# Kernel tuning notes

Hardware: AMD Instinct MI355X
Metric: run time of the kernel (lower is better)

## Reference

```python
import jax, jax.numpy as jnp
import numpy as np


def setup_inputs() -> dict:
    key = jax.random.key(0)
    k1, k2 = jax.random.split(key)
    B, C, N = 32, 512, 4096
    x = jax.random.normal(k1, (B, C, N), dtype=jnp.float32)
    gamma = jax.random.normal(k2, (1,), dtype=jnp.float32)
    return {"x": x, "gamma": gamma}


def reference(x, gamma):
    # x: [B, C, N]. Channel attention: energy = x @ x^T -> [B, C, C]
    energy = jnp.einsum('bcn,bdn->bcd', x, x)
    # inverted score: rowmax - energy, then softmax over last dim
    energy_new = jnp.max(energy, axis=-1, keepdims=True) - energy
    attention = jax.nn.softmax(energy_new, axis=-1)  # [B, C, C]
    out = jnp.einsum('bcd,bdn->bcn', attention, x)
    return gamma * out + x
```

## Files before the change

### kernel.cpp

```cpp
#include <hip/hip_runtime.h>
#include <stdint.h>
#include <stddef.h>

#define NB 32
#define NC 512
#define NN 4096
#define NSPLIT 4
#define KCH (NN / NSPLIT)

typedef _Float16 h4_t __attribute__((ext_vector_type(4)));
typedef _Float16 h8_t __attribute__((ext_vector_type(8)));
typedef float    f4_t __attribute__((ext_vector_type(4)));

__device__ __forceinline__ void gload16(const _Float16* g, _Float16* l) {
    __builtin_amdgcn_global_load_lds(
        (const __attribute__((address_space(1))) void*)g,
        (__attribute__((address_space(3))) void*)l, 16, 0, 0);
}

__global__ __launch_bounds__(256) void cast_hl(
    const float* __restrict__ x, _Float16* __restrict__ Xh,
    _Float16* __restrict__ Xl)
{
    const size_t total = (size_t)NB * NC * NN / 4;
    for (size_t i = (size_t)blockIdx.x * 256 + threadIdx.x; i < total;
         i += (size_t)gridDim.x * 256) {
        const float4 v = ((const float4*)x)[i];
        const _Float16 h0 = (_Float16)v.x, h1 = (_Float16)v.y;
        const _Float16 h2 = (_Float16)v.z, h3 = (_Float16)v.w;
        h4_t hv = {h0, h1, h2, h3};
        h4_t lv = {(_Float16)(v.x - (float)h0), (_Float16)(v.y - (float)h1),
                   (_Float16)(v.z - (float)h2), (_Float16)(v.w - (float)h3)};
        ((h4_t*)Xh)[i] = hv;
        ((h4_t*)Xl)[i] = lv;
    }
}

__global__ __launch_bounds__(256, 4) void gemm1_energy(
    const _Float16* __restrict__ Xh, const _Float16* __restrict__ Xl,
    float* __restrict__ part)
{
    __shared__ __attribute__((aligned(16))) _Float16 sAh[128 * 32];
    __shared__ __attribute__((aligned(16))) _Float16 sBh[128 * 32];
    __shared__ __attribute__((aligned(16))) _Float16 sAl[128 * 32];
    __shared__ __attribute__((aligned(16))) _Float16 sBl[128 * 32];

    const int flat = blockIdx.x;
    const int xcd  = flat & 7;
    const int slot = flat >> 3;
    const int grp  = xcd + 8 * (slot / 10);
    const int mem  = slot % 10;
    const int b    = grp >> 2;
    const int s    = grp & (NSPLIT - 1);

    const int ti = (int)((sqrtf(8.0f * (float)mem + 1.0f) - 1.0f) * 0.5f);
    const int tj = mem - ((ti * (ti + 1)) >> 1);

    const int t = threadIdx.x;
    const int wave = t >> 6, lane = t & 63;
    const int srow = t >> 2, scol = (t & 3) * 8;

    const size_t xb = (size_t)b * NC * NN + (size_t)s * KCH;
    const _Float16* gAh = Xh + xb + (size_t)(ti * 128 + srow) * NN + scol;
    const _Float16* gBh = Xh + xb + (size_t)(tj * 128 + srow) * NN + scol;
    const _Float16* gAl = Xl + xb + (size_t)(ti * 128 + srow) * NN + scol;
    const _Float16* gBl = Xl + xb + (size_t)(tj * 128 + srow) * NN + scol;

    const int wr = wave >> 1, wc = wave & 1;
    const int fr = lane & 15, fko = (lane >> 4) * 8;

    f4_t acc[4][4];
#pragma unroll
    for (int m = 0; m < 4; ++m)
#pragma unroll
        for (int n = 0; n < 4; ++n) acc[m][n] = (f4_t){0.f, 0.f, 0.f, 0.f};

    for (int k0 = 0; k0 < KCH; k0 += 32) {
        gload16(gAh + k0,                   sAh + wave * 512);
        gload16(gAh + k0 + 64 * (size_t)NN, sAh + 2048 + wave * 512);
        gload16(gBh + k0,                   sBh + wave * 512);
        gload16(gBh + k0 + 64 * (size_t)NN, sBh + 2048 + wave * 512);
        gload16(gAl + k0,                   sAl + wave * 512);
        gload16(gAl + k0 + 64 * (size_t)NN, sAl + 2048 + wave * 512);
        gload16(gBl + k0,                   sBl + wave * 512);
        gload16(gBl + k0 + 64 * (size_t)NN, sBl + 2048 + wave * 512);
        __syncthreads();

        h8_t ah[4], bh[4], al[4], bl[4];
#pragma unroll
        for (int m = 0; m < 4; ++m) {
            ah[m] = *(const h8_t*)(sAh + (wr * 64 + m * 16 + fr) * 32 + fko);
            bh[m] = *(const h8_t*)(sBh + (wc * 64 + m * 16 + fr) * 32 + fko);
            al[m] = *(const h8_t*)(sAl + (wr * 64 + m * 16 + fr) * 32 + fko);
            bl[m] = *(const h8_t*)(sBl + (wc * 64 + m * 16 + fr) * 32 + fko);
        }
#pragma unroll
        for (int m = 0; m < 4; ++m)
#pragma unroll
            for (int n = 0; n < 4; ++n) {
                acc[m][n] = __builtin_amdgcn_mfma_f32_16x16x32_f16(ah[m], bh[n], acc[m][n], 0, 0, 0);
                acc[m][n] = __builtin_amdgcn_mfma_f32_16x16x32_f16(ah[m], bl[n], acc[m][n], 0, 0, 0);
                acc[m][n] = __builtin_amdgcn_mfma_f32_16x16x32_f16(al[m], bh[n], acc[m][n], 0, 0, 0);
            }
        __syncthreads();
    }

    float* pb = part + ((size_t)s * NB + b) * (NC * NC);
    const int r0 = ti * 128 + wr * 64 + (lane >> 4) * 4;
    const int c0 = tj * 128 + wc * 64;
    const bool offdiag = (ti != tj);
#pragma unroll
    for (int m = 0; m < 4; ++m)
#pragma unroll
        for (int n = 0; n < 4; ++n) {
            const int col = c0 + n * 16 + fr;
#pragma unroll
            for (int j = 0; j < 4; ++j) {
                const int row = r0 + m * 16 + j;
                pb[(size_t)row * NC + col] = acc[m][n][j];
                if (offdiag) pb[(size_t)col * NC + row] = acc[m][n][j];
            }
        }
}

__global__ __launch_bounds__(256) void softmax_inv(
    const float* __restrict__ part, _Float16* __restrict__ attn)
{
    const int row = blockIdx.x * 4 + (threadIdx.x >> 6);
    const int lane = threadIdx.x & 63;
    const size_t roff = (size_t)row * NC;

    float4 a0 = {0.f, 0.f, 0.f, 0.f}, a1 = {0.f, 0.f, 0.f, 0.f};
#pragma unroll
    for (int s = 0; s < NSPLIT; ++s) {
        const float4* p = (const float4*)(part + (size_t)s * NB * NC * NC + roff);
        const float4 v0 = p[lane], v1 = p[64 + lane];
        a0.x += v0.x; a0.y += v0.y; a0.z += v0.z; a0.w += v0.w;
        a1.x += v1.x; a1.y += v1.y; a1.z += v1.z; a1.w += v1.w;
    }

    float mn = fminf(fminf(fminf(a0.x, a0.y), fminf(a0.z, a0.w)),
                     fminf(fminf(a1.x, a1.y), fminf(a1.z, a1.w)));
#pragma unroll
    for (int off = 32; off; off >>= 1) mn = fminf(mn, __shfl_xor(mn, off));

    const float w0 = __expf(mn - a0.x), w1 = __expf(mn - a0.y);
    const float w2 = __expf(mn - a0.z), w3 = __expf(mn - a0.w);
    const float w4 = __expf(mn - a1.x), w5 = __expf(mn - a1.y);
    const float w6 = __expf(mn - a1.z), w7 = __expf(mn - a1.w);
    float sum = ((w0 + w1) + (w2 + w3)) + ((w4 + w5) + (w6 + w7));
#pragma unroll
    for (int off = 32; off; off >>= 1) sum += __shfl_xor(sum, off);
    const float inv = 1.0f / sum;

    h4_t o0 = {(_Float16)(w0 * inv), (_Float16)(w1 * inv),
               (_Float16)(w2 * inv), (_Float16)(w3 * inv)};
    h4_t o1 = {(_Float16)(w4 * inv), (_Float16)(w5 * inv),
               (_Float16)(w6 * inv), (_Float16)(w7 * inv)};
    ((h4_t*)(attn + roff))[lane] = o0;
    ((h4_t*)(attn + roff))[64 + lane] = o1;
}

__global__ __launch_bounds__(256) void transpose_h(
    const _Float16* __restrict__ Xh, _Float16* __restrict__ Xt)
{
    __shared__ __attribute__((aligned(16))) _Float16 tile[64 * 66];
    const int b = blockIdx.z, c0 = blockIdx.y * 64, n0 = blockIdx.x * 64;
    const int t = threadIdx.x;
    const int lr = t >> 4;
    const int lc = (t & 15) * 4;
    const size_t hbase = (size_t)b * NC * NN;

#pragma unroll
    for (int p = 0; p < 4; ++p) {
        const int r = p * 16 + lr;
        const h4_t v = *(const h4_t*)(Xh + hbase + (size_t)(c0 + r) * NN + (n0 + lc));
        tile[r * 66 + lc + 0] = v[0];
        tile[r * 66 + lc + 1] = v[1];
        tile[r * 66 + lc + 2] = v[2];
        tile[r * 66 + lc + 3] = v[3];
    }
    __syncthreads();
    const size_t tbase = (size_t)b * NN * NC;
#pragma unroll
    for (int p = 0; p < 4; ++p) {
        const int rn = p * 16 + lr;
        h4_t w;
        w[0] = tile[(lc + 0) * 66 + rn];
        w[1] = tile[(lc + 1) * 66 + rn];
        w[2] = tile[(lc + 2) * 66 + rn];
        w[3] = tile[(lc + 3) * 66 + rn];
        *(h4_t*)(Xt + tbase + (size_t)(n0 + rn) * NC + (c0 + lc)) = w;
    }
}

__global__ __launch_bounds__(256) void gemm2_out(
    const _Float16* __restrict__ attn, const _Float16* __restrict__ Xt,
    const _Float16* __restrict__ Xh, const float* __restrict__ gammap,
    float* __restrict__ out)
{
    __shared__ __attribute__((aligned(16))) _Float16 sA[128 * 32];
    __shared__ __attribute__((aligned(16))) _Float16 sB[128 * 32];

    const int flat = blockIdx.x;
    const int xcd  = flat & 7;
    const int slot = flat >> 3;
    const int b    = xcd + 8 * (slot >> 7);
    const int memb = slot & 127;
    const int brow = (memb & 3) * 128;
    const int bcol = (memb >> 2) * 128;

    const int t = threadIdx.x;
    const int wave = t >> 6, lane = t & 63;
    const int srow = t >> 2, scol = (t & 3) * 8;

    const _Float16* gA = attn + (size_t)b * NC * NC + (size_t)(brow + srow) * NC + scol;
    const _Float16* gB = Xt   + (size_t)b * NN * NC + (size_t)(bcol + srow) * NC + scol;

    const int wr = wave >> 1, wc = wave & 1;
    const int fr = lane & 15, fko = (lane >> 4) * 8;

    f4_t acc[4][4];
#pragma unroll
    for (int m = 0; m < 4; ++m)
#pragma unroll
        for (int n = 0; n < 4; ++n) acc[m][n] = (f4_t){0.f, 0.f, 0.f, 0.f};

    for (int k0 = 0; k0 < NC; k0 += 32) {
        gload16(gA + k0,           sA + wave * 512);
        gload16(gA + k0 + 64 * NC, sA + 2048 + wave * 512);
        gload16(gB + k0,           sB + wave * 512);
        gload16(gB + k0 + 64 * NC, sB + 2048 + wave * 512);
        __syncthreads();

        h8_t a[4], bb[4];
#pragma unroll
        for (int m = 0; m < 4; ++m) {
            a[m]  = *(const h8_t*)(sA + (wr * 64 + m * 16 + fr) * 32 + fko);
            bb[m] = *(const h8_t*)(sB + (wc * 64 + m * 16 + fr) * 32 + fko);
        }
#pragma unroll
        for (int m = 0; m < 4; ++m)
#pragma unroll
            for (int n = 0; n < 4; ++n)
                acc[m][n] = __builtin_amdgcn_mfma_f32_16x16x32_f16(a[m], bb[n], acc[m][n], 0, 0, 0);
        __syncthreads();
    }

    const float g = gammap[0];
    const _Float16* xb = Xh + (size_t)b * NC * NN;
    float* ob = out + (size_t)b * NC * NN;
    const int r0 = brow + wr * 64 + (lane >> 4) * 4;
#pragma unroll
    for (int m = 0; m < 4; ++m)
#pragma unroll
        for (int n = 0; n < 4; ++n) {
            const int col = bcol + wc * 64 + n * 16 + fr;
#pragma unroll
            for (int j = 0; j < 4; ++j) {
                const int row = r0 + m * 16 + j;
                ob[(size_t)row * NN + col] =
                    g * acc[m][n][j] + (float)xb[(size_t)row * NN + col];
            }
        }
}

extern "C" void kernel_launch(void* const* d_in, const int* in_sizes, int n_in,
                              void* d_out, int out_size, void* d_ws, size_t ws_size,
                              hipStream_t stream)
{
    const float* x     = (const float*)d_in[0];
    const float* gamma = (const float*)d_in[1];
    float* out = (float*)d_out;
    char* ws = (char*)d_ws;

    _Float16* Xh   = (_Float16*)(ws);
    _Float16* XlXt = (_Float16*)(ws + 134217728ull);
    _Float16* attn = (_Float16*)(ws + 268435456ull);
    float*    part = (float*)   (ws + 285212672ull);

    cast_hl<<<dim3(2048), 256, 0, stream>>>(x, Xh, XlXt);

    gemm1_energy<<<dim3(10 * NSPLIT * NB), 256, 0, stream>>>(Xh, XlXt, part);

    softmax_inv<<<dim3(NB * NC / 4), 256, 0, stream>>>(part, attn);

    transpose_h<<<dim3(NN / 64, NC / 64, NB), 256, 0, stream>>>(Xh, XlXt);

    gemm2_out<<<dim3(4096), 256, 0, stream>>>(attn, XlXt, Xh, gamma, out);
}
```

Before: 512.6 us.

## Fuse cast with transpose, skip duplicate B loads on diagonal tiles, vectorize epilogues

Adds a cast_transpose kernel that writes the hi/lo fp16 splits and the transposed fp16 copy in one pass, removing the separate transpose kernel and its re-read of Xh. This path is used when the workspace is large enough. In gemm1, diagonal tiles read B from the A shared-memory buffers and skip the redundant B global loads. Both GEMMs swap MFMA operand order so each lane holds 4 consecutive columns, which allows vectorized float4 stores and half4 residual loads in the epilogues. The cost is a larger workspace requirement and a fallback path kept for smaller workspaces.

New measurement: 476.6 us. -7.0%, faster.

```diff
diff --git a/kernel.cpp b/kernel.cpp
--- a/kernel.cpp
+++ b/kernel.cpp
@@ -16,6 +16,48 @@
     __builtin_amdgcn_global_load_lds(
         (const __attribute__((address_space(1))) void*)g,
         (__attribute__((address_space(3))) void*)l, 16, 0, 0);
+}
+
+__global__ __launch_bounds__(256) void cast_transpose(
+    const float* __restrict__ x, _Float16* __restrict__ Xh,
+    _Float16* __restrict__ Xl, _Float16* __restrict__ Xt)
+{
+    __shared__ __attribute__((aligned(16))) _Float16 tile[64 * 66];
+    const int b = blockIdx.z, c0 = blockIdx.y * 64, n0 = blockIdx.x * 64;
+    const int t = threadIdx.x;
+    const int lr = t >> 4;
+    const int lc = (t & 15) * 4;
+    const size_t xbase = (size_t)b * NC * NN;
+
+#pragma unroll
+    for (int p = 0; p < 4; ++p) {
+        const int r = p * 16 + lr;
+        const size_t off = xbase + (size_t)(c0 + r) * NN + (n0 + lc);
+        const float4 v = *(const float4*)(x + off);
+        const _Float16 h0 = (_Float16)v.x, h1 = (_Float16)v.y;
+        const _Float16 h2 = (_Float16)v.z, h3 = (_Float16)v.w;
+        h4_t hv = {h0, h1, h2, h3};
+        *(h4_t*)(Xh + off) = hv;
+        h4_t lv = {(_Float16)(v.x - (float)h0), (_Float16)(v.y - (float)h1),
+                   (_Float16)(v.z - (float)h2), (_Float16)(v.w - (float)h3)};
+        *(h4_t*)(Xl + off) = lv;
+        tile[r * 66 + lc + 0] = h0;
+        tile[r * 66 + lc + 1] = h1;
+        tile[r * 66 + lc + 2] = h2;
+        tile[r * 66 + lc + 3] = h3;
+    }
+    __syncthreads();
+    const size_t tbase = (size_t)b * NN * NC;
+#pragma unroll
+    for (int p = 0; p < 4; ++p) {
+        const int rn = p * 16 + lr;
+        h4_t w;
+        w[0] = tile[(lc + 0) * 66 + rn];
+        w[1] = tile[(lc + 1) * 66 + rn];
+        w[2] = tile[(lc + 2) * 66 + rn];
+        w[3] = tile[(lc + 3) * 66 + rn];
+        *(h4_t*)(Xt + tbase + (size_t)(n0 + rn) * NC + (c0 + lc)) = w;
+    }
 }
 
 __global__ __launch_bounds__(256) void cast_hl(
@@ -55,6 +97,7 @@
 
     const int ti = (int)((sqrtf(8.0f * (float)mem + 1.0f) - 1.0f) * 0.5f);
     const int tj = mem - ((ti * (ti + 1)) >> 1);
+    const bool diag = (ti == tj);
 
     const int t = threadIdx.x;
     const int wave = t >> 6, lane = t & 63;
@@ -68,6 +111,10 @@
 
     const int wr = wave >> 1, wc = wave & 1;
     const int fr = lane & 15, fko = (lane >> 4) * 8;
+    const int hi4 = (lane >> 4) * 4;
+
+    const _Float16* rBh = diag ? sAh : sBh;
+    const _Float16* rBl = diag ? sAl : sBl;
 
     f4_t acc[4][4];
 #pragma unroll
@@ -78,49 +125,50 @@
     for (int k0 = 0; k0 < KCH; k0 += 32) {
         gload16(gAh + k0,                   sAh + wave * 512);
         gload16(gAh + k0 + 64 * (size_t)NN, sAh + 2048 + wave * 512);
-        gload16(gBh + k0,                   sBh + wave * 512);
-        gload16(gBh + k0 + 64 * (size_t)NN, sBh + 2048 + wave * 512);
         gload16(gAl + k0,                   sAl + wave * 512);
         gload16(gAl + k0 + 64 * (size_t)NN, sAl + 2048 + wave * 512);
-        gload16(gBl + k0,                   sBl + wave * 512);
-        gload16(gBl + k0 + 64 * (size_t)NN, sBl + 2048 + wave * 512);
+        if (!diag) {
+            gload16(gBh + k0,                   sBh + wave * 512);
+            gload16(gBh + k0 + 64 * (size_t)NN, sBh + 2048 + wave * 512);
+            gload16(gBl + k0,                   sBl + wave * 512);
+            gload16(gBl + k0 + 64 * (size_t)NN, sBl + 2048 + wave * 512);
+        }
         __syncthreads();
 
         h8_t ah[4], bh[4], al[4], bl[4];
 #pragma unroll
         for (int m = 0; m < 4; ++m) {
             ah[m] = *(const h8_t*)(sAh + (wr * 64 + m * 16 + fr) * 32 + fko);
-            bh[m] = *(const h8_t*)(sBh + (wc * 64 + m * 16 + fr) * 32 + fko);
+            bh[m] = *(const h8_t*)(rBh + (wc * 64 + m * 16 + fr) * 32 + fko);
             al[m] = *(const h8_t*)(sAl + (wr * 64 + m * 16 + fr) * 32 + fko);
-            bl[m] = *(const h8_t*)(sBl + (wc * 64 + m * 16 + fr) * 32 + fko);
+            bl[m] = *(const h8_t*)(rBl + (wc * 64 + m * 16 + fr) * 32 + fko);
         }
 #pragma unroll
         for (int m = 0; m < 4; ++m)
 #pragma unroll
-            for (int n = 0; n < 4; ++n) {
-                acc[m][n] = __builtin_amdgcn_mfma_f32_16x16x32_f16(ah[m], bh[n], acc[m][n], 0, 0, 0);
-                acc[m][n] = __builtin_amdgcn_mfma_f32_16x16x32_f16(ah[m], bl[n], acc[m][n], 0, 0, 0);
-                acc[m][n] = __builtin_amdgcn_mfma_f32_16x16x32_f16(al[m], bh[n], acc[m][n], 0, 0, 0);
+            for (int nf = 0; nf < 4; ++nf) {
+                acc[nf][m] = __builtin_amdgcn_mfma_f32_16x16x32_f16(bh[nf], ah[m], acc[nf][m], 0, 0, 0);
+                acc[nf][m] = __builtin_amdgcn_mfma_f32_16x16x32_f16(bl[nf], ah[m], acc[nf][m], 0, 0, 0);
+                acc[nf][m] = __builtin_amdgcn_mfma_f32_16x16x32_f16(bh[nf], al[m], acc[nf][m], 0, 0, 0);
             }
         __syncthreads();
     }
 
     float* pb = part + ((size_t)s * NB + b) * (NC * NC);
-    const int r0 = ti * 128 + wr * 64 + (lane >> 4) * 4;
-    const int c0 = tj * 128 + wc * 64;
-    const bool offdiag = (ti != tj);
-#pragma unroll
-    for (int m = 0; m < 4; ++m)
-#pragma unroll
-        for (int n = 0; n < 4; ++n) {
-            const int col = c0 + n * 16 + fr;
-#pragma unroll
-            for (int j = 0; j < 4; ++j) {
-                const int row = r0 + m * 16 + j;
-                pb[(size_t)row * NC + col] = acc[m][n][j];
-                if (offdiag) pb[(size_t)col * NC + row] = acc[m][n][j];
+#pragma unroll
+    for (int m = 0; m < 4; ++m) {
+        const int i = ti * 128 + wr * 64 + m * 16 + fr;
+#pragma unroll
+        for (int nf = 0; nf < 4; ++nf) {
+            const int jjb = tj * 128 + wc * 64 + nf * 16 + hi4;
+            *(f4_t*)(pb + (size_t)i * NC + jjb) = acc[nf][m];
+            if (!diag) {
+#pragma unroll
+                for (int j = 0; j < 4; ++j)
+                    pb[(size_t)(jjb + j) * NC + i] = acc[nf][m][j];
             }
         }
+    }
 }
 
 __global__ __launch_bounds__(256) void softmax_inv(
@@ -219,6 +267,7 @@
 
     const int wr = wave >> 1, wc = wave & 1;
     const int fr = lane & 15, fko = (lane >> 4) * 8;
+    const int hi4 = (lane >> 4) * 4;
 
     f4_t acc[4][4];
 #pragma unroll
@@ -242,27 +291,29 @@
 #pragma unroll
         for (int m = 0; m < 4; ++m)
 #pragma unroll
-            for (int n = 0; n < 4; ++n)
-                acc[m][n] = __builtin_amdgcn_mfma_f32_16x16x32_f16(a[m], bb[n], acc[m][n], 0, 0, 0);
+            for (int nf = 0; nf < 4; ++nf)
+                acc[nf][m] = __builtin_amdgcn_mfma_f32_16x16x32_f16(bb[nf], a[m], acc[nf][m], 0, 0, 0);
         __syncthreads();
     }
 
     const float g = gammap[0];
     const _Float16* xb = Xh + (size_t)b * NC * NN;
     float* ob = out + (size_t)b * NC * NN;
-    const int r0 = brow + wr * 64 + (lane >> 4) * 4;
-#pragma unroll
-    for (int m = 0; m < 4; ++m)
-#pragma unroll
-        for (int n = 0; n < 4; ++n) {
-            const int col = bcol + wc * 64 + n * 16 + fr;
-#pragma unroll
-            for (int j = 0; j < 4; ++j) {
-                const int row = r0 + m * 16 + j;
-                ob[(size_t)row * NN + col] =
-                    g * acc[m][n][j] + (float)xb[(size_t)row * NN + col];
-            }
-        }
+#pragma unroll
+    for (int m = 0; m < 4; ++m) {
+        const int c_ = brow + wr * 64 + m * 16 + fr;
+#pragma unroll
+        for (int nf = 0; nf < 4; ++nf) {
+            const int n_ = bcol + wc * 64 + nf * 16 + hi4;
+            const size_t off = (size_t)c_ * NN + n_;
+            const h4_t xv = *(const h4_t*)(xb + off);
+            f4_t o;
+#pragma unroll
+            for (int j = 0; j < 4; ++j)
+                o[j] = g * acc[nf][m][j] + (float)xv[j];
+            *(f4_t*)(ob + off) = o;
+        }
+    }
 }
 
 extern "C" void kernel_launch(void* const* d_in, const int* in_sizes, int n_in,
@@ -274,18 +325,27 @@
     float* out = (float*)d_out;
     char* ws = (char*)d_ws;
 
-    _Float16* Xh   = (_Float16*)(ws);
-    _Float16* XlXt = (_Float16*)(ws + 134217728ull);
-    _Float16* attn = (_Float16*)(ws + 268435456ull);
-    float*    part = (float*)   (ws + 285212672ull);
-
-    cast_hl<<<dim3(2048), 256, 0, stream>>>(x, Xh, XlXt);
-
-    gemm1_energy<<<dim3(10 * NSPLIT * NB), 256, 0, stream>>>(Xh, XlXt, part);
-
-    softmax_inv<<<dim3(NB * NC / 4), 256, 0, stream>>>(part, attn);
-
-    transpose_h<<<dim3(NN / 64, NC / 64, NB), 256, 0, stream>>>(Xh, XlXt);
-
-    gemm2_out<<<dim3(4096), 256, 0, stream>>>(attn, XlXt, Xh, gamma, out);
-}
+    if (ws_size >= 553648128ull) {
+        _Float16* Xh   = (_Float16*)(ws);
+        _Float16* Xl   = (_Float16*)(ws + 134217728ull);
+        _Float16* Xt   = (_Float16*)(ws + 268435456ull);
+        _Float16* attn = (_Float16*)(ws + 402653184ull);
+        float*    part = (float*)   (ws + 419430400ull);
+
+        cast_transpose<<<dim3(NN / 64, NC / 64, NB), 256, 0, stream>>>(x, Xh, Xl, Xt);
+        gemm1_energy<<<dim3(10 * NSPLIT * NB), 256, 0, stream>>>(Xh, Xl, part);
+        softmax_inv<<<dim3(NB * NC / 4), 256, 0, stream>>>(part, attn);
+        gemm2_out<<<dim3(4096), 256, 0, stream>>>(attn, Xt, Xh, gamma, out);
+    } else {
+        _Float16* Xh   = (_Float16*)(ws);
+        _Float16* XlXt = (_Float16*)(ws + 134217728ull);
+        _Float16* attn = (_Float16*)(ws + 268435456ull);
+        float*    part = (float*)   (ws + 285212672ull);
+
+        cast_hl<<<dim3(2048), 256, 0, stream>>>(x, Xh, XlXt);
+        gemm1_energy<<<dim3(10 * NSPLIT * NB), 256, 0, stream>>>(Xh, XlXt, part);
+        softmax_inv<<<dim3(NB * NC / 4), 256, 0, stream>>>(part, attn);
+        transpose_h<<<dim3(NN / 64, NC / 64, NB), 256, 0, stream>>>(Xh, XlXt);
+        gemm2_out<<<dim3(4096), 256, 0, stream>>>(attn, XlXt, Xh, gamma, out);
+    }
+}
```
